# Kernel optimization log

Hardware: AMD Instinct MI355X
Metric: run time of the kernel (lower is better)

## Reference

```python
import jax, jax.numpy as jnp
import numpy as np

B, L, E, H = 8, 256, 256, 8
A = E // H
LEAKAGE = 0.2


def setup_inputs() -> dict:
    key = jax.random.key(0)
    k1, k2, k3, k4, k5 = jax.random.split(key, 5)
    embeddings = jax.random.normal(k1, (B, L, E), dtype=jnp.float32)
    adj = jax.random.bernoulli(k2, 0.5, (B, L, L))
    # guarantee self-loops so no row is fully masked
    adj = adj | jnp.eye(L, dtype=bool)[None]
    s = 1.0 / np.sqrt(E)
    W_qk = jax.random.normal(k3, (2 * E, E), dtype=jnp.float32) * s   # torch Linear weight [out,in]
    w_attn = jax.random.normal(k4, (A,), dtype=jnp.float32) * (1.0 / np.sqrt(A))
    W_out = jax.random.normal(k5, (E, E), dtype=jnp.float32) * s
    return {"embeddings": embeddings, "adj": adj, "W_qk": W_qk, "w_attn": w_attn, "W_out": W_out}


def reference(embeddings, adj, W_qk, w_attn, W_out):
    Bc, Lc, Ec = embeddings.shape
    qk = embeddings @ W_qk.T                      # [B,L,2E]
    qk = qk.reshape(Bc, Lc, H, 2 * A).transpose(0, 2, 1, 3)  # [B,H,L,2A]
    q, k = qk[..., :A], qk[..., A:]               # [B,H,L,A] each
    # attn[b,h,i,j,:] = q[b,h,j] + k[b,h,i]
    s = q[:, :, None, :, :] + k[:, :, :, None, :]  # [B,H,L,L,A]
    s = jnp.where(s >= 0, s, LEAKAGE * s)          # LeakyReLU
    scores = jnp.einsum('bhija,a->bhij', s, w_attn)
    neg = jnp.finfo(scores.dtype).min
    scores = jnp.where(adj[:, None, :, :], scores, neg)
    attn = jax.nn.softmax(scores, axis=-1)         # over j
    vals = jnp.einsum('bhij,bhja->bhia', attn, k)  # [B,H,L,A]
    vals = vals.transpose(0, 2, 1, 3).reshape(Bc, Lc, Ec)
    return vals @ W_out.T
```

## Files before the change

### kernel.cpp

```cpp
#include <hip/hip_runtime.h>
#include <hip/hip_bf16.h>
#include <math.h>

#define B_ 8
#define L_ 256
#define E_ 256
#define H_ 8
#define A_ 32
#define ITILE 32

typedef __attribute__((ext_vector_type(8))) short bf16x8;
typedef __attribute__((ext_vector_type(4))) float f32x4;

__device__ __forceinline__ int swz(int row, int slot) {
  return row * 128 + ((slot ^ (row & 7)) << 4);
}

__device__ __forceinline__ void pack8(const float4& x, const float4& y,
                                      bf16x8& h, bf16x8& l) {
  float v[8] = {x.x, x.y, x.z, x.w, y.x, y.y, y.z, y.w};
  union { __hip_bfloat16 b[8]; bf16x8 v; } uh, ul;
#pragma unroll
  for (int i = 0; i < 8; ++i) {
    uh.b[i] = __float2bfloat16(v[i]);
    ul.b[i] = __float2bfloat16(v[i] - __bfloat162float(uh.b[i]));
  }
  h = uh.v;
  l = ul.v;
}

template <int MODE>
__global__ __launch_bounds__(256) void gemm_mfma(const float* __restrict__ Ag,
                                                 const float* __restrict__ Bg,
                                                 float* __restrict__ C0,
                                                 float* __restrict__ C1,
                                                 int N) {
  __shared__ __align__(16) char lds[4 * 8192];
  char* Ah = lds;
  char* Al = lds + 8192;
  char* Bh = lds + 16384;
  char* Bl = lds + 24576;

  const int ntile = N >> 6;
  const int mt = blockIdx.x / ntile;
  const int nt = blockIdx.x % ntile;
  const int t = threadIdx.x;
  const int wave = t >> 6, lane = t & 63;
  const int wr = wave >> 1, wc = wave & 1;
  const int r15 = lane & 15, g4 = lane >> 4;
  const int srow = t >> 2, sq = t & 3;

  f32x4 acc[2][2];
#pragma unroll
  for (int rb = 0; rb < 2; ++rb)
#pragma unroll
    for (int cb = 0; cb < 2; ++cb) acc[rb][cb] = (f32x4){0.f, 0.f, 0.f, 0.f};

  for (int kt = 0; kt < 256; kt += 64) {
    const float4* ap4 =
        (const float4*)(Ag + (mt * 64 + srow) * 256 + kt + sq * 16);
    const float4* bp4 =
        (const float4*)(Bg + (nt * 64 + srow) * 256 + kt + sq * 16);
    float4 a0 = ap4[0], a1 = ap4[1], a2 = ap4[2], a3 = ap4[3];
    float4 b0 = bp4[0], b1 = bp4[1], b2 = bp4[2], b3 = bp4[3];
    bf16x8 h, l;
    pack8(a0, a1, h, l);
    *(bf16x8*)(Ah + swz(srow, 2 * sq)) = h;
    *(bf16x8*)(Al + swz(srow, 2 * sq)) = l;
    pack8(a2, a3, h, l);
    *(bf16x8*)(Ah + swz(srow, 2 * sq + 1)) = h;
    *(bf16x8*)(Al + swz(srow, 2 * sq + 1)) = l;
    pack8(b0, b1, h, l);
    *(bf16x8*)(Bh + swz(srow, 2 * sq)) = h;
    *(bf16x8*)(Bl + swz(srow, 2 * sq)) = l;
    pack8(b2, b3, h, l);
    *(bf16x8*)(Bh + swz(srow, 2 * sq + 1)) = h;
    *(bf16x8*)(Bl + swz(srow, 2 * sq + 1)) = l;
    __syncthreads();

    bf16x8 fah[2][2], fal[2][2], fbh[2][2], fbl[2][2];
#pragma unroll
    for (int rb = 0; rb < 2; ++rb)
#pragma unroll
      for (int ks = 0; ks < 2; ++ks) {
        int slot = 4 * ks + g4;
        int arow = wr * 32 + rb * 16 + r15;
        fah[rb][ks] = *(const bf16x8*)(Ah + swz(arow, slot));
        fal[rb][ks] = *(const bf16x8*)(Al + swz(arow, slot));
        int brow = wc * 32 + rb * 16 + r15;
        fbh[rb][ks] = *(const bf16x8*)(Bh + swz(brow, slot));
        fbl[rb][ks] = *(const bf16x8*)(Bl + swz(brow, slot));
      }
#pragma unroll
    for (int rb = 0; rb < 2; ++rb)
#pragma unroll
      for (int cb = 0; cb < 2; ++cb)
#pragma unroll
        for (int ks = 0; ks < 2; ++ks) {
          acc[rb][cb] = __builtin_amdgcn_mfma_f32_16x16x32_bf16(
              fal[rb][ks], fbh[cb][ks], acc[rb][cb], 0, 0, 0);
          acc[rb][cb] = __builtin_amdgcn_mfma_f32_16x16x32_bf16(
              fah[rb][ks], fbl[cb][ks], acc[rb][cb], 0, 0, 0);
          acc[rb][cb] = __builtin_amdgcn_mfma_f32_16x16x32_bf16(
              fah[rb][ks], fbh[cb][ks], acc[rb][cb], 0, 0, 0);
        }
    __syncthreads();
  }

#pragma unroll
  for (int rb = 0; rb < 2; ++rb)
#pragma unroll
    for (int cb = 0; cb < 2; ++cb)
#pragma unroll
      for (int g = 0; g < 4; ++g) {
        int gr = mt * 64 + wr * 32 + rb * 16 + g4 * 4 + g;
        int gc = nt * 64 + wc * 32 + cb * 16 + r15;
        if (MODE == 0) {
          C0[gr * N + gc] = acc[rb][cb][g];
        } else {
          int b = gr >> 8, lrow = gr & 255;
          int x = gc & 63;
          float* dst = (x < A_) ? C0 : C1;
          dst[((b * H_ + nt) * L_ + lrow) * A_ + (x & 31)] = acc[rb][cb][g];
        }
      }
}

__global__ __launch_bounds__(256, 2) void attn_kernel(
    const float* __restrict__ q, const float* __restrict__ k,
    const int* __restrict__ adj, const float* __restrict__ w_attn,
    float* __restrict__ vals) {
  __shared__ __align__(16) float Qt[A_][260];
  __shared__ __align__(16) __hip_bfloat16 KT[A_][264];
  __shared__ __align__(16) float Kr[ITILE][36];
  __shared__ __align__(16) __hip_bfloat16 S[ITILE][264];
  __shared__ __align__(16) float wsh[A_];

  const int bh = blockIdx.x >> 3;
  const int it = blockIdx.x & 7;
  const int b = bh >> 3, h = bh & 7;
  const int t = threadIdx.x;

  const float4* qb4 = (const float4*)(q + bh * (L_ * A_));
  const float4* kb4 = (const float4*)(k + bh * (L_ * A_));
#pragma unroll
  for (int r = 0; r < 8; ++r) {
    int idx4 = r * 256 + t;
    int j = idx4 >> 3, ab = idx4 & 7;
    float4 v = qb4[idx4];
    Qt[ab * 4 + 0][j] = v.x;
    Qt[ab * 4 + 1][j] = v.y;
    Qt[ab * 4 + 2][j] = v.z;
    Qt[ab * 4 + 3][j] = v.w;
    float4 u = kb4[idx4];
    KT[ab * 4 + 0][j] = __float2bfloat16(u.x);
    KT[ab * 4 + 1][j] = __float2bfloat16(u.y);
    KT[ab * 4 + 2][j] = __float2bfloat16(u.z);
    KT[ab * 4 + 3][j] = __float2bfloat16(u.w);
  }
  {
    const float4* kr4g = (const float4*)(k + bh * (L_ * A_) + it * ITILE * A_);
    int ii = t >> 3, ab = t & 7;
    float4 v = kr4g[t];
    Kr[ii][ab * 4 + 0] = v.x;
    Kr[ii][ab * 4 + 1] = v.y;
    Kr[ii][ab * 4 + 2] = v.z;
    Kr[ii][ab * 4 + 3] = v.w;
  }
  if (t < A_) wsh[t] = w_attn[t];
  __syncthreads();

  const int wave = t >> 6, lane = t & 63;
  const int w8 = wave * 8;
  const int i0 = it * ITILE + w8;
  const int* adjb = adj + b * (L_ * L_);

  int adjv[8][4];
#pragma unroll
  for (int r = 0; r < 8; ++r)
#pragma unroll
    for (int c = 0; c < 4; ++c)
      adjv[r][c] = adjb[(i0 + r) * L_ + c * 64 + lane];

  float p[8][4] = {};
  float ck[8] = {};
  float cq[4] = {};
#pragma unroll 2
  for (int ab = 0; ab < 8; ++ab) {
    float4 wv = *(const float4*)&wsh[ab * 4];
    float4 kr4[8];
#pragma unroll
    for (int r = 0; r < 8; ++r)
      kr4[r] = *(const float4*)&Kr[w8 + r][ab * 4];
#pragma unroll
    for (int r = 0; r < 8; ++r) {
      ck[r] = fmaf(wv.x, kr4[r].x, ck[r]);
      ck[r] = fmaf(wv.y, kr4[r].y, ck[r]);
      ck[r] = fmaf(wv.z, kr4[r].z, ck[r]);
      ck[r] = fmaf(wv.w, kr4[r].w, ck[r]);
    }
#pragma unroll
    for (int c = 0; c < 4; ++c) {
      const int j = c * 64 + lane;
      float q0 = Qt[ab * 4 + 0][j];
      float q1 = Qt[ab * 4 + 1][j];
      float q2 = Qt[ab * 4 + 2][j];
      float q3 = Qt[ab * 4 + 3][j];
      cq[c] = fmaf(wv.x, q0, cq[c]);
      cq[c] = fmaf(wv.y, q1, cq[c]);
      cq[c] = fmaf(wv.z, q2, cq[c]);
      cq[c] = fmaf(wv.w, q3, cq[c]);
#pragma unroll
      for (int r = 0; r < 8; ++r) {
        p[r][c] = fmaf(wv.x, fabsf(kr4[r].x + q0), p[r][c]);
        p[r][c] = fmaf(wv.y, fabsf(kr4[r].y + q1), p[r][c]);
        p[r][c] = fmaf(wv.z, fabsf(kr4[r].z + q2), p[r][c]);
        p[r][c] = fmaf(wv.w, fabsf(kr4[r].w + q3), p[r][c]);
      }
    }
  }

#pragma unroll
  for (int r = 0; r < 8; ++r) {
    float s[4];
    float m = -3.0e38f;
#pragma unroll
    for (int c = 0; c < 4; ++c) {
      float sc = fmaf(0.4f, p[r][c], 0.6f * (ck[r] + cq[c]));
      s[c] = adjv[r][c] ? sc : -3.0e38f;
      m = fmaxf(m, s[c]);
    }
#pragma unroll
    for (int off = 32; off >= 1; off >>= 1) m = fmaxf(m, __shfl_xor(m, off));
    float sum = 0.f;
#pragma unroll
    for (int c = 0; c < 4; ++c) {
      s[c] = __expf(s[c] - m);
      sum += s[c];
    }
#pragma unroll
    for (int off = 32; off >= 1; off >>= 1) sum += __shfl_xor(sum, off);
    float inv = 1.0f / sum;
#pragma unroll
    for (int c = 0; c < 4; ++c)
      S[w8 + r][c * 64 + lane] = __float2bfloat16(s[c] * inv);
  }
  __syncthreads();

  const int mi = wave >> 1;
  const int ai = wave & 1;
  const int fr = lane & 15;
  const int fk = (lane >> 4) * 8;
  f32x4 acc = {0.f, 0.f, 0.f, 0.f};
#pragma unroll
  for (int kt = 0; kt < 8; ++kt) {
    bf16x8 afrag = *(const bf16x8*)&S[mi * 16 + fr][kt * 32 + fk];
    bf16x8 bfrag = *(const bf16x8*)&KT[ai * 16 + fr][kt * 32 + fk];
    acc = __builtin_amdgcn_mfma_f32_16x16x32_bf16(afrag, bfrag, acc, 0, 0, 0);
  }
  const int arow = ai * 16 + fr;
  const int rbase = mi * 16 + ((lane >> 4) << 2);
#pragma unroll
  for (int g = 0; g < 4; ++g) {
    int i = it * ITILE + rbase + g;
    vals[(b * L_ + i) * E_ + h * A_ + arow] = acc[g];
  }
}

extern "C" void kernel_launch(void* const* d_in, const int* in_sizes, int n_in,
                              void* d_out, int out_size, void* d_ws,
                              size_t ws_size, hipStream_t stream) {
  const float* emb = (const float*)d_in[0];
  const int* adj = (const int*)d_in[1];
  const float* W_qk = (const float*)d_in[2];
  const float* w_attn = (const float*)d_in[3];
  const float* W_out = (const float*)d_in[4];
  float* out = (float*)d_out;

  float* q = (float*)d_ws;
  float* k = q + B_ * H_ * L_ * A_;
  float* vals = k + B_ * H_ * L_ * A_;

  gemm_mfma<1><<<dim3(32 * 8), 256, 0, stream>>>(emb, W_qk, q, k, 512);
  attn_kernel<<<dim3(B_ * H_ * (L_ / ITILE)), 256, 0, stream>>>(q, k, adj,
                                                                w_attn, vals);
  gemm_mfma<0><<<dim3(32 * 4), 256, 0, stream>>>(vals, W_out, out, nullptr,
                                                 256);
}
```

Before: 98.74 us.

## Fuse QK GEMM, attention and output GEMM into one cooperative kernel

New measurement: 260.7 us. 2.64x slower.

```diff
diff --git a/kernel.cpp b/kernel.cpp
--- a/kernel.cpp
+++ b/kernel.cpp
@@ -1,16 +1,20 @@
 #include <hip/hip_runtime.h>
+#include <hip/hip_cooperative_groups.h>
 #include <hip/hip_bf16.h>
 #include <math.h>
+
+namespace cg = cooperative_groups;
 
 #define B_ 8
 #define L_ 256
 #define E_ 256
 #define H_ 8
 #define A_ 32
-#define ITILE 32
 
 typedef __attribute__((ext_vector_type(8))) short bf16x8;
 typedef __attribute__((ext_vector_type(4))) float f32x4;
+
+#define SMEM_BYTES 93312
 
 __device__ __forceinline__ int swz(int row, int slot) {
   return row * 128 + ((slot ^ (row & 7)) << 4);
@@ -30,122 +34,109 @@
 }
 
 template <int MODE>
-__global__ __launch_bounds__(256) void gemm_mfma(const float* __restrict__ Ag,
-                                                 const float* __restrict__ Bg,
-                                                 float* __restrict__ C0,
-                                                 float* __restrict__ C1,
-                                                 int N) {
-  __shared__ __align__(16) char lds[4 * 8192];
+__device__ void gemm_body(char* lds, const float* __restrict__ Ag,
+                          const float* __restrict__ Bg, float* __restrict__ C0,
+                          float* __restrict__ C1, int N, int bid) {
   char* Ah = lds;
   char* Al = lds + 8192;
   char* Bh = lds + 16384;
   char* Bl = lds + 24576;
 
   const int ntile = N >> 6;
-  const int mt = blockIdx.x / ntile;
-  const int nt = blockIdx.x % ntile;
+  const int mt = bid / ntile;
+  const int nt = bid % ntile;
   const int t = threadIdx.x;
   const int wave = t >> 6, lane = t & 63;
-  const int wr = wave >> 1, wc = wave & 1;
+  const int wr = wave >> 2, wc = wave & 3;
   const int r15 = lane & 15, g4 = lane >> 4;
-  const int srow = t >> 2, sq = t & 3;
-
-  f32x4 acc[2][2];
-#pragma unroll
-  for (int rb = 0; rb < 2; ++rb)
-#pragma unroll
-    for (int cb = 0; cb < 2; ++cb) acc[rb][cb] = (f32x4){0.f, 0.f, 0.f, 0.f};
+  const int srow = t >> 3, slot = t & 7;
+
+  f32x4 acc[2];
+  acc[0] = (f32x4){0.f, 0.f, 0.f, 0.f};
+  acc[1] = (f32x4){0.f, 0.f, 0.f, 0.f};
 
   for (int kt = 0; kt < 256; kt += 64) {
     const float4* ap4 =
-        (const float4*)(Ag + (mt * 64 + srow) * 256 + kt + sq * 16);
+        (const float4*)(Ag + (mt * 64 + srow) * 256 + kt + slot * 8);
     const float4* bp4 =
-        (const float4*)(Bg + (nt * 64 + srow) * 256 + kt + sq * 16);
-    float4 a0 = ap4[0], a1 = ap4[1], a2 = ap4[2], a3 = ap4[3];
-    float4 b0 = bp4[0], b1 = bp4[1], b2 = bp4[2], b3 = bp4[3];
+        (const float4*)(Bg + (nt * 64 + srow) * 256 + kt + slot * 8);
+    float4 a0 = ap4[0], a1 = ap4[1];
+    float4 b0 = bp4[0], b1 = bp4[1];
     bf16x8 h, l;
     pack8(a0, a1, h, l);
-    *(bf16x8*)(Ah + swz(srow, 2 * sq)) = h;
-    *(bf16x8*)(Al + swz(srow, 2 * sq)) = l;
-    pack8(a2, a3, h, l);
-    *(bf16x8*)(Ah + swz(srow, 2 * sq + 1)) = h;
-    *(bf16x8*)(Al + swz(srow, 2 * sq + 1)) = l;
+    *(bf16x8*)(Ah + swz(srow, slot)) = h;
+    *(bf16x8*)(Al + swz(srow, slot)) = l;
     pack8(b0, b1, h, l);
-    *(bf16x8*)(Bh + swz(srow, 2 * sq)) = h;
-    *(bf16x8*)(Bl + swz(srow, 2 * sq)) = l;
-    pack8(b2, b3, h, l);
-    *(bf16x8*)(Bh + swz(srow, 2 * sq + 1)) = h;
-    *(bf16x8*)(Bl + swz(srow, 2 * sq + 1)) = l;
+    *(bf16x8*)(Bh + swz(srow, slot)) = h;
+    *(bf16x8*)(Bl + swz(srow, slot)) = l;
     __syncthreads();
 
-    bf16x8 fah[2][2], fal[2][2], fbh[2][2], fbl[2][2];
+    bf16x8 fah[2][2], fal[2][2], fbh[2], fbl[2];
+#pragma unroll
+    for (int ks = 0; ks < 2; ++ks) {
+      int sl = 4 * ks + g4;
+#pragma unroll
+      for (int rb = 0; rb < 2; ++rb) {
+        int arow = wr * 32 + rb * 16 + r15;
+        fah[rb][ks] = *(const bf16x8*)(Ah + swz(arow, sl));
+        fal[rb][ks] = *(const bf16x8*)(Al + swz(arow, sl));
+      }
+      int brow = wc * 16 + r15;
+      fbh[ks] = *(const bf16x8*)(Bh + swz(brow, sl));
+      fbl[ks] = *(const bf16x8*)(Bl + swz(brow, sl));
+    }
 #pragma unroll
     for (int rb = 0; rb < 2; ++rb)
 #pragma unroll
       for (int ks = 0; ks < 2; ++ks) {
-        int slot = 4 * ks + g4;
-        int arow = wr * 32 + rb * 16 + r15;
-        fah[rb][ks] = *(const bf16x8*)(Ah + swz(arow, slot));
-        fal[rb][ks] = *(const bf16x8*)(Al + swz(arow, slot));
-        int brow = wc * 32 + rb * 16 + r15;
-        fbh[rb][ks] = *(const bf16x8*)(Bh + swz(brow, slot));
-        fbl[rb][ks] = *(const bf16x8*)(Bl + swz(brow, slot));
+        acc[rb] = __builtin_amdgcn_mfma_f32_16x16x32_bf16(fal[rb][ks], fbh[ks],
+                                                          acc[rb], 0, 0, 0);
+        acc[rb] = __builtin_amdgcn_mfma_f32_16x16x32_bf16(fah[rb][ks], fbl[ks],
+                                                          acc[rb], 0, 0, 0);
+        acc[rb] = __builtin_amdgcn_mfma_f32_16x16x32_bf16(fah[rb][ks], fbh[ks],
+                                                          acc[rb], 0, 0, 0);
       }
-#pragma unroll
-    for (int rb = 0; rb < 2; ++rb)
-#pragma unroll
-      for (int cb = 0; cb < 2; ++cb)
-#pragma unroll
-        for (int ks = 0; ks < 2; ++ks) {
-          acc[rb][cb] = __builtin_amdgcn_mfma_f32_16x16x32_bf16(
-              fal[rb][ks], fbh[cb][ks], acc[rb][cb], 0, 0, 0);
-          acc[rb][cb] = __builtin_amdgcn_mfma_f32_16x16x32_bf16(
-              fah[rb][ks], fbl[cb][ks], acc[rb][cb], 0, 0, 0);
-          acc[rb][cb] = __builtin_amdgcn_mfma_f32_16x16x32_bf16(
-              fah[rb][ks], fbh[cb][ks], acc[rb][cb], 0, 0, 0);
-        }
     __syncthreads();
   }
 
 #pragma unroll
   for (int rb = 0; rb < 2; ++rb)
 #pragma unroll
-    for (int cb = 0; cb < 2; ++cb)
-#pragma unroll
-      for (int g = 0; g < 4; ++g) {
-        int gr = mt * 64 + wr * 32 + rb * 16 + g4 * 4 + g;
-        int gc = nt * 64 + wc * 32 + cb * 16 + r15;
-        if (MODE == 0) {
-          C0[gr * N + gc] = acc[rb][cb][g];
-        } else {
-          int b = gr >> 8, lrow = gr & 255;
-          int x = gc & 63;
-          float* dst = (x < A_) ? C0 : C1;
-          dst[((b * H_ + nt) * L_ + lrow) * A_ + (x & 31)] = acc[rb][cb][g];
-        }
+    for (int g = 0; g < 4; ++g) {
+      int gr = mt * 64 + wr * 32 + rb * 16 + g4 * 4 + g;
+      int gc = nt * 64 + wc * 16 + r15;
+      if (MODE == 0) {
+        C0[gr * N + gc] = acc[rb][g];
+      } else {
+        int b = gr >> 8, lrow = gr & 255;
+        int hh = gc >> 6, x = gc & 63;
+        float* dst = (x < A_) ? C0 : C1;
+        dst[((b * H_ + hh) * L_ + lrow) * A_ + (x & 31)] = acc[rb][g];
       }
-}
-
-__global__ __launch_bounds__(256, 2) void attn_kernel(
-    const float* __restrict__ q, const float* __restrict__ k,
-    const int* __restrict__ adj, const float* __restrict__ w_attn,
-    float* __restrict__ vals) {
-  __shared__ __align__(16) float Qt[A_][260];
-  __shared__ __align__(16) __hip_bfloat16 KT[A_][264];
-  __shared__ __align__(16) float Kr[ITILE][36];
-  __shared__ __align__(16) __hip_bfloat16 S[ITILE][264];
-  __shared__ __align__(16) float wsh[A_];
-
-  const int bh = blockIdx.x >> 3;
-  const int it = blockIdx.x & 7;
+    }
+}
+
+__device__ void attn_body(char* smem, const float* __restrict__ q,
+                          const float* __restrict__ k,
+                          const int* __restrict__ adj,
+                          const float* __restrict__ w_attn,
+                          float* __restrict__ vals, int bid) {
+  float(*Qt)[260] = (float(*)[260])smem;
+  __hip_bfloat16(*KT)[264] = (__hip_bfloat16(*)[264])(smem + 33280);
+  float(*Kr)[36] = (float(*)[36])(smem + 50176);
+  __hip_bfloat16(*S)[264] = (__hip_bfloat16(*)[264])(smem + 59392);
+  float* wsh = (float*)(smem + 93184);
+
+  const int bh = bid >> 2;
+  const int it = bid & 3;
   const int b = bh >> 3, h = bh & 7;
   const int t = threadIdx.x;
 
   const float4* qb4 = (const float4*)(q + bh * (L_ * A_));
   const float4* kb4 = (const float4*)(k + bh * (L_ * A_));
 #pragma unroll
-  for (int r = 0; r < 8; ++r) {
-    int idx4 = r * 256 + t;
+  for (int r = 0; r < 4; ++r) {
+    int idx4 = r * 512 + t;
     int j = idx4 >> 3, ab = idx4 & 7;
     float4 v = qb4[idx4];
     Qt[ab * 4 + 0][j] = v.x;
@@ -159,7 +150,7 @@
     KT[ab * 4 + 3][j] = __float2bfloat16(u.w);
   }
   {
-    const float4* kr4g = (const float4*)(k + bh * (L_ * A_) + it * ITILE * A_);
+    const float4* kr4g = (const float4*)(k + bh * (L_ * A_) + it * 64 * A_);
     int ii = t >> 3, ab = t & 7;
     float4 v = kr4g[t];
     Kr[ii][ab * 4 + 0] = v.x;
@@ -172,7 +163,7 @@
 
   const int wave = t >> 6, lane = t & 63;
   const int w8 = wave * 8;
-  const int i0 = it * ITILE + w8;
+  const int i0 = it * 64 + w8;
   const int* adjb = adj + b * (L_ * L_);
 
   int adjv[8][4];
@@ -262,9 +253,29 @@
   const int rbase = mi * 16 + ((lane >> 4) << 2);
 #pragma unroll
   for (int g = 0; g < 4; ++g) {
-    int i = it * ITILE + rbase + g;
+    int i = it * 64 + rbase + g;
     vals[(b * L_ + i) * E_ + h * A_ + arow] = acc[g];
   }
+}
+
+__global__ __launch_bounds__(512, 1) void gat_fused(
+    const float* __restrict__ emb, const int* __restrict__ adj,
+    const float* __restrict__ W_qk, const float* __restrict__ w_attn,
+    const float* __restrict__ W_out, float* __restrict__ out,
+    float* __restrict__ q, float* __restrict__ k, float* __restrict__ vals) {
+  __shared__ __align__(16) char smem[SMEM_BYTES];
+  cg::grid_group grid = cg::this_grid();
+  const int bid = blockIdx.x;
+
+  gemm_body<1>(smem, emb, W_qk, q, k, 512, bid);
+  __threadfence();
+  grid.sync();
+
+  attn_body(smem, q, k, adj, w_attn, vals, bid);
+  __threadfence();
+  grid.sync();
+
+  if (bid < 128) gemm_body<0>(smem, vals, W_out, out, nullptr, 256, bid);
 }
 
 extern "C" void kernel_launch(void* const* d_in, const int* in_sizes, int n_in,
@@ -281,9 +292,9 @@
   float* k = q + B_ * H_ * L_ * A_;
   float* vals = k + B_ * H_ * L_ * A_;
 
-  gemm_mfma<1><<<dim3(32 * 8), 256, 0, stream>>>(emb, W_qk, q, k, 512);
-  attn_kernel<<<dim3(B_ * H_ * (L_ / ITILE)), 256, 0, stream>>>(q, k, adj,
-                                                                w_attn, vals);
-  gemm_mfma<0><<<dim3(32 * 4), 256, 0, stream>>>(vals, W_out, out, nullptr,
-                                                 256);
-}
+  void* args[] = {(void*)&emb, (void*)&adj,   (void*)&W_qk,
+                  (void*)&w_attn, (void*)&W_out, (void*)&out,
+                  (void*)&q,   (void*)&k,     (void*)&vals};
+  hipLaunchCooperativeKernel((void*)gat_fused, dim3(256), dim3(512), args, 0,
+                             stream);
+}
```
